# Kernel tuning notes

Hardware: AMD Instinct MI355X
Metric: run time of the kernel (lower is better)

Reference implementation:

```python
import jax, jax.numpy as jnp
import numpy as np

B, S, D, H = 2, 2048, 1024, 16
HD = D // H  # 64


def setup_inputs() -> dict:
    key = jax.random.key(0)
    ks = jax.random.split(key, 7)
    scale = 1.0 / np.sqrt(D)
    return {
        "embeddings": jax.random.normal(ks[0], (B, S, D), dtype=jnp.float32),
        "W_kv": jax.random.uniform(ks[1], (D, 2 * D), jnp.float32, -scale, scale),
        "b_kv": jax.random.uniform(ks[2], (2 * D,), jnp.float32, -scale, scale),
        "W_q": jax.random.uniform(ks[3], (D, D), jnp.float32, -scale, scale),
        "b_q": jax.random.uniform(ks[4], (D,), jnp.float32, -scale, scale),
        "W_o": jax.random.uniform(ks[5], (D, D), jnp.float32, -scale, scale),
        "b_o": jax.random.uniform(ks[6], (D,), jnp.float32, -scale, scale),
    }


def reference(embeddings, W_kv, b_kv, W_q, b_q, W_o, b_o):
    # kv projection -> [B, S, H, 2*HD] -> [B, H, S, 2*HD]
    kv = (embeddings @ W_kv + b_kv).reshape(B, S, H, 2 * HD).transpose(0, 2, 1, 3)
    q = (embeddings @ W_q + b_q).reshape(B, S, H, HD).transpose(0, 2, 1, 3)
    k, v = kv[..., :HD], kv[..., HD:]
    # naive scaled dot-product attention (full [B,H,S,S] score matrix)
    scores = jnp.einsum("bhqd,bhkd->bhqk", q, k) / jnp.sqrt(jnp.float32(HD))
    attn = jax.nn.softmax(scores, axis=-1)
    ctx = jnp.einsum("bhqk,bhkd->bhqd", attn, v)  # [B,H,S,HD]
    ctx = ctx.transpose(0, 2, 1, 3).reshape(B, S, D)
    return ctx @ W_o + b_o
```

## Files before the change

kernel.cpp:

```cpp
#include <hip/hip_runtime.h>
#include <hip/hip_bf16.h>


typedef unsigned short ushort;
typedef __attribute__((ext_vector_type(4))) float f32x4;
typedef __attribute__((ext_vector_type(16))) float f32x16;
typedef __attribute__((ext_vector_type(8))) __bf16 bf16x8;
typedef __attribute__((ext_vector_type(8))) unsigned short u16x8;
typedef __attribute__((ext_vector_type(4))) unsigned short u16x4;
typedef __attribute__((ext_vector_type(4))) unsigned int u32x4;

#define LOG2E 1.44269504088896340736f

constexpr int Bc = 2, Sc = 2048, Dc = 1024, Hc = 16, HDc = 64;

__device__ inline ushort f2bf(float f) {
    unsigned u = __builtin_bit_cast(unsigned, f);
    u += 0x7fffu + ((u >> 16) & 1u);
    return (ushort)(u >> 16);
}

__device__ inline float fexp2(float x) {
#if __has_builtin(__builtin_amdgcn_exp2f)
    return __builtin_amdgcn_exp2f(x);
#else
    return exp2f(x);
#endif
}

__device__ inline void gload16(const void* g, void* l) {
    __builtin_amdgcn_global_load_lds((const __attribute__((address_space(1))) void*)g,
                                     (__attribute__((address_space(3))) void*)l, 16, 0, 0);
}

__device__ inline f32x4 mfma16(bf16x8 a, bf16x8 b, f32x4 c) {
    return __builtin_amdgcn_mfma_f32_16x16x32_bf16(a, b, c, 0, 0, 0);
}
__device__ inline f32x16 mfma32(bf16x8 a, bf16x8 b, f32x16 c) {
    return __builtin_amdgcn_mfma_f32_32x32x16_bf16(a, b, c, 0, 0, 0);
}
__device__ inline unsigned cvtpk(float lo, float hi_) {
    unsigned r; asm("v_cvt_pk_bf16_f32 %0, %1, %2" : "=v"(r) : "v"(lo), "v"(hi_)); return r;
}
__device__ inline void swap32(unsigned& a, unsigned& b) {
    asm("v_permlane32_swap_b32 %0, %1" : "+v"(a), "+v"(b));
}

__global__ __launch_bounds__(256) void prep_k(const float* __restrict__ emb,
                                              ushort* __restrict__ embb,
                                              const float* __restrict__ Wkv,
                                              const float* __restrict__ Wq,
                                              const float* __restrict__ Wo,
                                              ushort* __restrict__ WtAll) {
    const int bid = blockIdx.x;
    if (bid < 2048) {
        int i = bid * 256 + threadIdx.x;
        const float4* p = (const float4*)emb;
        float4 a = p[2 * i], b = p[2 * i + 1];
        u16x8 r;
        r[0] = f2bf(a.x); r[1] = f2bf(a.y); r[2] = f2bf(a.z); r[3] = f2bf(a.w);
        r[4] = f2bf(b.x); r[5] = f2bf(b.y); r[6] = f2bf(b.z); r[7] = f2bf(b.w);
        ((u16x8*)embb)[i] = r;
        return;
    }
    __shared__ float t[32][33];
    int tb = bid - 2048;
    const float* W; int N, rowofs;
    if (tb < 2048)      { W = Wkv; N = 2048; rowofs = 0; }
    else if (tb < 3072) { W = Wq;  N = 1024; rowofs = 2048; tb -= 2048; }
    else                { W = Wo;  N = 1024; rowofs = 3072; tb -= 3072; }
    const int nbx = N >> 5;
    const int bx = tb % nbx, by = tb / nbx;
    const int tx = threadIdx.x & 31, ty = threadIdx.x >> 5;
    const int bj = bx * 32, bi = by * 32;
#pragma unroll
    for (int i = 0; i < 4; i++) {
        int r = ty + i * 8;
        t[r][tx] = W[(size_t)(bi + r) * N + bj + tx];
    }
    __syncthreads();
#pragma unroll
    for (int i = 0; i < 4; i++) {
        int r = ty + i * 8;
        WtAll[(size_t)(rowofs + bj + r) * 1024 + bi + tx] = f2bf(t[tx][r]);
    }
}

__global__ __launch_bounds__(512, 2) void gemm256_kv_k(const ushort* __restrict__ A,
                                                       const ushort* __restrict__ Bt,
                                                       const float* __restrict__ bias,
                                                       const float* __restrict__ bias2,
                                                       ushort* __restrict__ Kout,
                                                       ushort* __restrict__ Vout,
                                                       ushort* __restrict__ Qout,
                                                       int N, int K) {
    __shared__ __align__(16) char sA[2][32768];
    __shared__ __align__(16) char sB[2][32768];
    const int tid = threadIdx.x;
    const int nbc = N >> 8;
    const int cpx = (gridDim.x >> 3);
    const int swzb = (blockIdx.x & 7) * cpx + (blockIdx.x >> 3);
    const int brow = swzb / nbc, bcol = swzb % nbc;
    const int w = tid >> 6, lane = tid & 63;
    const int wr = w >> 2, wc = w & 3;
    const int lg = lane >> 4, l16 = lane & 15;

    f32x4 acc[8][4] = {};

    const int srow = tid >> 3;
    const int schunk = (tid & 7) ^ (srow & 7);
    const ushort* aP[4];
    const ushort* bP[4];
#pragma unroll
    for (int s = 0; s < 4; s++) {
        aP[s] = A  + (size_t)(brow * 256 + s * 64 + srow) * K + schunk * 8;
        bP[s] = Bt + (size_t)(bcol * 256 + s * 64 + srow) * K + schunk * 8;
    }

    auto STAGE_ALL = [&](int buf, int k0) {
#pragma unroll
        for (int s = 0; s < 4; s++)
            gload16(aP[s] + k0, sA[buf] + s * 8192 + w * 1024);
#pragma unroll
        for (int s = 0; s < 4; s++)
            gload16(bP[s] + k0, sB[buf] + s * 8192 + w * 1024);
    };

    const int aro = wr * 128 + l16;
    const int bro = wc * 64 + l16;
    const int axor = l16 & 7;

    const int nk = K >> 6;
    STAGE_ALL(0, 0);

    for (int kt = 0; kt < nk; kt++) {
        const int buf = kt & 1;
        if (kt < nk - 1) {
            STAGE_ALL(buf ^ 1, (kt + 1) << 6);
            asm volatile("s_waitcnt vmcnt(8)" ::: "memory");
        } else {
            asm volatile("s_waitcnt vmcnt(0)" ::: "memory");
        }
        __builtin_amdgcn_s_barrier();
        __builtin_amdgcn_sched_barrier(0);

#pragma unroll
        for (int ks = 0; ks < 2; ks++) {
            bf16x8 af[8], bfr[4];
#pragma unroll
            for (int rf = 0; rf < 8; rf++)
                af[rf] = *(const bf16x8*)(sA[buf] + (aro + rf * 16) * 128 +
                                          ((((ks << 2) | lg) ^ axor) << 4));
#pragma unroll
            for (int cf = 0; cf < 4; cf++)
                bfr[cf] = *(const bf16x8*)(sB[buf] + (bro + cf * 16) * 128 +
                                           ((((ks << 2) | lg) ^ axor) << 4));
#pragma unroll
            for (int rf = 0; rf < 8; rf++)
#pragma unroll
                for (int cf = 0; cf < 4; cf++)
                    acc[rf][cf] = mfma16(af[rf], bfr[cf], acc[rf][cf]);
        }
        __builtin_amdgcn_s_barrier();
    }

#pragma unroll
    for (int cf = 0; cf < 4; cf++) {
        const int col = bcol * 256 + wc * 64 + cf * 16 + l16;
        if (col < 2048) {
            const float bv = bias[col];
            const int h = col >> 7, lo = col & 127;
#pragma unroll
            for (int rf = 0; rf < 8; rf++) {
                int row = brow * 256 + wr * 128 + rf * 16 + lg * 4;
                int b = row >> 11, s = row & 2047;
                if (lo < 64) {
#pragma unroll
                    for (int r = 0; r < 4; r++)
                        Kout[((size_t)(b * 16 + h) * 2048 + s + r) * 64 + lo] =
                            f2bf(acc[rf][cf][r] + bv);
                } else {
                    u16x4 pk;
#pragma unroll
                    for (int r = 0; r < 4; r++) pk[r] = f2bf(acc[rf][cf][r] + bv);
                    *(u16x4*)(Vout + ((size_t)(b * 16 + h) * 64 + (lo - 64)) * 2048 + s) = pk;
                }
            }
        } else {
            const int qc = col - 2048;
            const float bv = bias2[qc];
            const float qs = 0.125f * LOG2E;
#pragma unroll
            for (int rf = 0; rf < 8; rf++) {
                int row = brow * 256 + wr * 128 + rf * 16 + lg * 4;
#pragma unroll
                for (int r = 0; r < 4; r++)
                    Qout[(size_t)(row + r) * 1024 + qc] =
                        f2bf((acc[rf][cf][r] + bv) * qs);
            }
        }
    }
}

template <int MODE>
__global__ __launch_bounds__(256) void gemm_bt_k(const ushort* __restrict__ A,
                                                 const ushort* __restrict__ Bt,
                                                 const float* __restrict__ bias,
                                                 void* __restrict__ Cout,
                                                 int M, int N, int K) {
    __shared__ __align__(16) char sA[2][8192];
    __shared__ __align__(16) char sB[2][8192];
    const int tid = threadIdx.x;
    const int nbc = N >> 7;
    const int cpx = (gridDim.x >> 3);
    const int swzb = (blockIdx.x & 7) * cpx + (blockIdx.x >> 3);
    const int brow = swzb / nbc, bcol = swzb % nbc;
    const int w = tid >> 6, lane = tid & 63;
    const int wr = w >> 1, wc = w & 1;
    const int lg = lane >> 4, l16 = lane & 15;

    f32x4 acc[4][4] = {};

    const int r0 = tid >> 2;
    const int sl = (tid & 3) ^ (r0 & 3);
    const ushort* a0 = A + (size_t)(brow * 128 + r0) * K + sl * 8;
    const ushort* a1 = A + (size_t)(brow * 128 + 64 + r0) * K + sl * 8;
    const ushort* b0 = Bt + (size_t)(bcol * 128 + r0) * K + sl * 8;
    const ushort* b1 = Bt + (size_t)(bcol * 128 + 64 + r0) * K + sl * 8;

    const int arow = wr * 64 + l16;
    const int bcolr = wc * 64 + l16;

    auto STAGE = [&](int buf, int k0) {
        gload16(a0 + k0, sA[buf] + w * 1024);
        gload16(a1 + k0, sA[buf] + 4096 + w * 1024);
        gload16(b0 + k0, sB[buf] + w * 1024);
        gload16(b1 + k0, sB[buf] + 4096 + w * 1024);
    };

    const int nk = K >> 5;
    STAGE(0, 0);

    for (int k0 = 0; k0 < nk; k0++) {
        const int buf = k0 & 1;
        if (k0 < nk - 1) {
            STAGE(buf ^ 1, (k0 + 1) << 5);
            asm volatile("s_waitcnt vmcnt(4)" ::: "memory");
        } else {
            asm volatile("s_waitcnt vmcnt(0)" ::: "memory");
        }
        __builtin_amdgcn_s_barrier();
        __builtin_amdgcn_sched_barrier(0);

        bf16x8 af[4], bfr[4];
#pragma unroll
        for (int rf = 0; rf < 4; rf++) {
            int rr = arow + rf * 16;
            af[rf] = *(const bf16x8*)(sA[buf] + rr * 64 + ((lg * 16) ^ ((rr & 3) << 4)));
        }
#pragma unroll
        for (int cf = 0; cf < 4; cf++) {
            int rr = bcolr + cf * 16;
            bfr[cf] = *(const bf16x8*)(sB[buf] + rr * 64 + ((lg * 16) ^ ((rr & 3) << 4)));
        }
#pragma unroll
        for (int rf = 0; rf < 4; rf++)
#pragma unroll
            for (int cf = 0; cf < 4; cf++)
                acc[rf][cf] = mfma16(af[rf], bfr[cf], acc[rf][cf]);
        __builtin_amdgcn_s_barrier();
    }

#pragma unroll
    for (int cf = 0; cf < 4; cf++) {
        const int col = bcol * 128 + wc * 64 + cf * 16 + l16;
        const float bv = bias[col];
#pragma unroll
        for (int rf = 0; rf < 4; rf++) {
            int row = brow * 128 + wr * 64 + rf * 16 + lg * 4;
#pragma unroll
            for (int r = 0; r < 4; r++) {
                float v = acc[rf][cf][r] + bv;
                if (MODE == 1) ((float*)Cout)[(size_t)(row + r) * N + col] = v;
                else           ((ushort*)Cout)[(size_t)(row + r) * N + col] = f2bf(v);
            }
        }
    }
}

__global__ __launch_bounds__(256, 2) void attn2_k(const ushort* __restrict__ Qg,
                                                  const ushort* __restrict__ Kg,
                                                  const ushort* __restrict__ Vg,
                                                  ushort* __restrict__ ctx) {
    __shared__ __align__(16) char sK[2][8192];
    __shared__ __align__(16) char sV[2][8192];
    __shared__ float lx2[256];
    const int tid = threadIdx.x;
    const int wg = ((blockIdx.x & 7) << 6) | (blockIdx.x >> 3);
    const int bh = wg >> 4, qt = wg & 15;
    const int b = bh >> 4, h = bh & 15;
    const int w = tid >> 6, lane = tid & 63;
    const int ql = lane & 31, hi = lane >> 5;
    const int ksub = w & 1;
    const int qq = w >> 1;

    const ushort* Kh = Kg + (size_t)bh * (Sc * 64);
    const ushort* Vh = Vg + (size_t)bh * (64 * Sc);

    const int qrow0 = qt * 128 + qq * 64 + ql;
    bf16x8 qf[2][4];
#pragma unroll
    for (int qg = 0; qg < 2; qg++) {
        const ushort* qp = Qg + ((size_t)(b * Sc + qrow0 + qg * 32)) * Dc + h * HDc + hi * 8;
#pragma unroll
        for (int jd = 0; jd < 4; jd++) qf[qg][jd] = *(const bf16x8*)(qp + jd * 16);
    }

    const u16x8 ones_u = {0x3F80, 0x3F80, 0x3F80, 0x3F80, 0x3F80, 0x3F80, 0x3F80, 0x3F80};
    const bf16x8 ones8 = __builtin_bit_cast(bf16x8, ones_u);

    const int rw = w * 16 + (lane >> 3);
    const int sl = (lane & 7) ^ (lane >> 3);

    f32x16 o[2][2] = {};
    f32x16 ls[2] = {};
    const float MH = 8.0f * LOG2E;
    const int sw = (ql & 7) << 4;

    auto STAGE = [&](int buf, int kt) {
#pragma unroll
        for (int j = 0; j < 2; j++) {
            gload16(Kh + (size_t)(kt * 64 + rw + 8 * j) * 64 + sl * 8,
                    sK[buf] + w * 2048 + j * 1024);
            gload16(Vh + (size_t)(rw + 8 * j) * Sc + kt * 64 + sl * 8,
                    sV[buf] + w * 2048 + j * 1024);
        }
    };

    int cur = 0;
    STAGE(0, 0);

    constexpr int NT = Sc / 64;
    for (int kt = 0; kt < NT; kt++) {
        if (kt < NT - 1) {
            STAGE(cur ^ 1, kt + 1);
            asm volatile("s_waitcnt vmcnt(4)" ::: "memory");
        } else {
            asm volatile("s_waitcnt vmcnt(0)" ::: "memory");
        }
        __builtin_amdgcn_s_barrier();
        __builtin_amdgcn_sched_barrier(0);

        bf16x8 kf[4];
        {
            const char* kb = sK[cur] + (ksub * 32 + ql) * 128;
#pragma unroll
            for (int jd = 0; jd < 4; jd++)
                kf[jd] = *(const bf16x8*)(kb + ((jd * 32 + hi * 16) ^ sw));
        }

        f32x16 st[2];
#pragma unroll
        for (int qg = 0; qg < 2; qg++)
#pragma unroll
            for (int i = 0; i < 16; i++) st[qg][i] = -MH;
        __builtin_amdgcn_s_setprio(1);
#pragma unroll
        for (int qg = 0; qg < 2; qg++)
#pragma unroll
            for (int jd = 0; jd < 4; jd++)
                st[qg] = mfma32(kf[jd], qf[qg][jd], st[qg]);
        __builtin_amdgcn_s_setprio(0);

#pragma unroll
        for (int qg = 0; qg < 2; qg++)
#pragma unroll
            for (int i = 0; i < 16; i++) st[qg][i] = fexp2(st[qg][i]);

        bf16x8 pf[2][2];
#pragma unroll
        for (int qg = 0; qg < 2; qg++) {
            unsigned a0 = cvtpk(st[qg][0],  st[qg][1]);
            unsigned a1 = cvtpk(st[qg][2],  st[qg][3]);
            unsigned a2 = cvtpk(st[qg][4],  st[qg][5]);
            unsigned a3 = cvtpk(st[qg][6],  st[qg][7]);
            swap32(a0, a2); swap32(a1, a3);
            u32x4 f0v = {a0, a1, a2, a3};
            pf[qg][0] = __builtin_bit_cast(bf16x8, f0v);
            unsigned c0 = cvtpk(st[qg][8],  st[qg][9]);
            unsigned c1 = cvtpk(st[qg][10], st[qg][11]);
            unsigned c2 = cvtpk(st[qg][12], st[qg][13]);
            unsigned c3 = cvtpk(st[qg][14], st[qg][15]);
            swap32(c0, c2); swap32(c1, c3);
            u32x4 f1v = {c0, c1, c2, c3};
            pf[qg][1] = __builtin_bit_cast(bf16x8, f1v);
        }

        bf16x8 vf[2][2];
#pragma unroll
        for (int dg = 0; dg < 2; dg++) {
            const char* vb = sV[cur] + (dg * 32 + ql) * 128;
#pragma unroll
            for (int ks = 0; ks < 2; ks++)
                vf[dg][ks] = *(const bf16x8*)(vb + ((ksub * 64 + ks * 32 + hi * 16) ^ sw));
        }

        __builtin_amdgcn_s_setprio(1);
#pragma unroll
        for (int qg = 0; qg < 2; qg++)
#pragma unroll
            for (int ks = 0; ks < 2; ks++) {
                o[0][qg] = mfma32(vf[0][ks], pf[qg][ks], o[0][qg]);
                o[1][qg] = mfma32(vf[1][ks], pf[qg][ks], o[1][qg]);
                ls[qg]   = mfma32(ones8,     pf[qg][ks], ls[qg]);
            }
        __builtin_amdgcn_s_setprio(0);

        __builtin_amdgcn_s_barrier();
        cur ^= 1;
    }

    __syncthreads();
    float* ox = qq ? (float*)sV : (float*)sK;
    if (ksub) {
#pragma unroll
        for (int dg = 0; dg < 2; dg++)
#pragma unroll
            for (int qg = 0; qg < 2; qg++)
#pragma unroll
                for (int i = 0; i < 16; i++)
                    ox[((dg * 2 + qg) * 16 + i) * 64 + lane] = o[dg][qg][i];
        lx2[(qq * 2 + 0) * 64 + lane] = ls[0][0];
        lx2[(qq * 2 + 1) * 64 + lane] = ls[1][0];
    }
    __syncthreads();
    if (!ksub) {
#pragma unroll
        for (int dg = 0; dg < 2; dg++)
#pragma unroll
            for (int qg = 0; qg < 2; qg++)
#pragma unroll
                for (int i = 0; i < 16; i++)
                    o[dg][qg][i] += ox[((dg * 2 + qg) * 16 + i) * 64 + lane];
        const float inv0 = 1.0f / (ls[0][0] + lx2[(qq * 2 + 0) * 64 + lane]);
        const float inv1 = 1.0f / (ls[1][0] + lx2[(qq * 2 + 1) * 64 + lane]);
#pragma unroll
        for (int qg = 0; qg < 2; qg++) {
            const float inv = qg ? inv1 : inv0;
            ushort* cp = ctx + ((size_t)(b * Sc + qrow0 + qg * 32)) * Dc + h * HDc;
#pragma unroll
            for (int dg = 0; dg < 2; dg++)
#pragma unroll
                for (int g = 0; g < 4; g++) {
                    u16x4 pk;
#pragma unroll
                    for (int r = 0; r < 4; r++)
                        pk[r] = f2bf(o[dg][qg][g * 4 + r] * inv);
                    *(u16x4*)(cp + dg * 32 + g * 8 + hi * 4) = pk;
                }
        }
    }
}

extern "C" void kernel_launch(void* const* d_in, const int* in_sizes, int n_in,
                              void* d_out, int out_size, void* d_ws, size_t ws_size,
                              hipStream_t stream) {
    const float* emb  = (const float*)d_in[0];
    const float* W_kv = (const float*)d_in[1];
    const float* b_kv = (const float*)d_in[2];
    const float* W_q  = (const float*)d_in[3];
    const float* b_q  = (const float*)d_in[4];
    const float* W_o  = (const float*)d_in[5];
    const float* b_o  = (const float*)d_in[6];
    float* out = (float*)d_out;

    const int BS = Bc * Sc;
    ushort* embb  = (ushort*)d_ws;
    ushort* wallt = embb  + (size_t)BS * Dc;
    ushort* wot   = wallt + (size_t)3 * Dc * Dc;
    ushort* Kb    = wallt + (size_t)4 * Dc * Dc;
    ushort* Vtb   = Kb    + (size_t)32 * Sc * HDc;
    ushort* Qb    = Vtb   + (size_t)32 * Sc * HDc;
    ushort* ctxb  = Qb    + (size_t)BS * Dc;

    prep_k<<<6144, 256, 0, stream>>>(emb, embb, W_kv, W_q, W_o, wallt);

    gemm256_kv_k<<<(BS / 256) * (3072 / 256), 512, 0, stream>>>(
        embb, wallt, b_kv, b_q, Kb, Vtb, Qb, 3072, Dc);

    attn2_k<<<Bc * Hc * (Sc / 128), 256, 0, stream>>>(Qb, Kb, Vtb, ctxb);

    gemm_bt_k<1><<<(BS / 128) * (Dc / 128), 256, 0, stream>>>(
        ctxb, wot, b_o, out, BS, Dc, Dc);
}
```

Measured before the change: 118.9 us.

## Restructure QKV GEMM mainloop into 8-phase quarter-tile ping-pong pipeline

The 256x256 QKV projection GEMM's main loop is split into four sub-phases, each working on half of A and half of B. In each phase the LDS fragment loads, the global-to-LDS prefetch for a quarter tile two iterations ahead, and a block of MFMAs are interleaved, with s_setprio around the MFMA groups. This aims to hide global load latency and LDS reads behind matrix math instead of stalling at one barrier per k-tile. In exchange there are many more barriers and tricky buffer reuse: quarters of the current buffer are overwritten while other quarters are still being consumed, which relies on careful ordering.

Measured after the change: 119.1 us. About the same (+0.1%).

```diff
diff --git a/kernel.cpp b/kernel.cpp
--- a/kernel.cpp
+++ b/kernel.cpp
@@ -86,14 +86,14 @@
     }
 }
 
-__global__ __launch_bounds__(512, 2) void gemm256_kv_k(const ushort* __restrict__ A,
-                                                       const ushort* __restrict__ Bt,
-                                                       const float* __restrict__ bias,
-                                                       const float* __restrict__ bias2,
-                                                       ushort* __restrict__ Kout,
-                                                       ushort* __restrict__ Vout,
-                                                       ushort* __restrict__ Qout,
-                                                       int N, int K) {
+__global__ __launch_bounds__(512, 2) void gemm256_kv8_k(const ushort* __restrict__ A,
+                                                        const ushort* __restrict__ Bt,
+                                                        const float* __restrict__ bias,
+                                                        const float* __restrict__ bias2,
+                                                        ushort* __restrict__ Kout,
+                                                        ushort* __restrict__ Vout,
+                                                        ushort* __restrict__ Qout,
+                                                        int N, int K) {
     __shared__ __align__(16) char sA[2][32768];
     __shared__ __align__(16) char sB[2][32768];
     const int tid = threadIdx.x;
@@ -104,64 +104,103 @@
     const int w = tid >> 6, lane = tid & 63;
     const int wr = w >> 2, wc = w & 3;
     const int lg = lane >> 4, l16 = lane & 15;
+    const int lx7 = l16 & 7;
 
     f32x4 acc[8][4] = {};
 
-    const int srow = tid >> 3;
-    const int schunk = (tid & 7) ^ (srow & 7);
-    const ushort* aP[4];
-    const ushort* bP[4];
-#pragma unroll
-    for (int s = 0; s < 4; s++) {
-        aP[s] = A  + (size_t)(brow * 256 + s * 64 + srow) * K + schunk * 8;
-        bP[s] = Bt + (size_t)(bcol * 256 + s * 64 + srow) * K + schunk * 8;
-    }
-
-    auto STAGE_ALL = [&](int buf, int k0) {
-#pragma unroll
-        for (int s = 0; s < 4; s++)
-            gload16(aP[s] + k0, sA[buf] + s * 8192 + w * 1024);
-#pragma unroll
-        for (int s = 0; s < 4; s++)
-            gload16(bP[s] + k0, sB[buf] + s * 8192 + w * 1024);
-    };
-
-    const int aro = wr * 128 + l16;
-    const int bro = wc * 64 + l16;
-    const int axor = l16 & 7;
+    const int srow8 = lane >> 3;
+    const int sch = (lane & 7) ^ srow8;
+    const ushort* Ab = A  + (size_t)(brow * 256 + w * 8 + srow8) * K + sch * 8;
+    const ushort* Bb = Bt + (size_t)(bcol * 256 + (w >> 2) * 64 + (w & 3) * 8 + srow8) * K + sch * 8;
+
+    auto ST_A = [&](int buf, int mh, int k0) {
+#pragma unroll
+        for (int j = 0; j < 2; j++)
+            gload16(Ab + (size_t)(j * 128 + mh * 64) * K + k0,
+                    sA[buf] + mh * 16384 + j * 8192 + w * 1024);
+    };
+    auto ST_B = [&](int buf, int nh, int k0) {
+#pragma unroll
+        for (int j = 0; j < 2; j++)
+            gload16(Bb + (size_t)(j * 128 + nh * 32) * K + k0,
+                    sB[buf] + nh * 16384 + j * 8192 + w * 1024);
+    };
+
+    bf16x8 af[4][2], bfr[2][2];
+    auto LD_A = [&](int buf, int mh) {
+#pragma unroll
+        for (int rf = 0; rf < 4; rf++)
+#pragma unroll
+            for (int ks = 0; ks < 2; ks++)
+                af[rf][ks] = *(const bf16x8*)(sA[buf] + mh * 16384 + wr * 8192 +
+                             (rf * 16 + l16) * 128 + ((((ks << 2) | lg) ^ lx7) << 4));
+    };
+    auto LD_B = [&](int buf, int nh) {
+#pragma unroll
+        for (int cf = 0; cf < 2; cf++)
+#pragma unroll
+            for (int ks = 0; ks < 2; ks++)
+                bfr[cf][ks] = *(const bf16x8*)(sB[buf] + nh * 16384 + wc * 4096 +
+                              (cf * 16 + l16) * 128 + ((((ks << 2) | lg) ^ lx7) << 4));
+    };
+    auto MMA = [&](int mh, int nh) {
+        __builtin_amdgcn_s_setprio(1);
+#pragma unroll
+        for (int rf = 0; rf < 4; rf++)
+#pragma unroll
+            for (int cf = 0; cf < 2; cf++)
+#pragma unroll
+                for (int ks = 0; ks < 2; ks++)
+                    acc[mh * 4 + rf][nh * 2 + cf] =
+                        mfma16(af[rf][ks], bfr[cf][ks], acc[mh * 4 + rf][nh * 2 + cf]);
+        __builtin_amdgcn_s_setprio(0);
+    };
 
     const int nk = K >> 6;
-    STAGE_ALL(0, 0);
+    ST_A(0, 0, 0);  ST_B(0, 1, 0);  ST_A(0, 1, 0);  ST_B(0, 0, 0);
+    ST_A(1, 0, 64); ST_B(1, 1, 64); ST_A(1, 1, 64);
+    asm volatile("s_waitcnt vmcnt(6)" ::: "memory");
+    __builtin_amdgcn_s_barrier();
+    __builtin_amdgcn_sched_barrier(0);
 
     for (int kt = 0; kt < nk; kt++) {
         const int buf = kt & 1;
-        if (kt < nk - 1) {
-            STAGE_ALL(buf ^ 1, (kt + 1) << 6);
-            asm volatile("s_waitcnt vmcnt(8)" ::: "memory");
-        } else {
-            asm volatile("s_waitcnt vmcnt(0)" ::: "memory");
-        }
-        __builtin_amdgcn_s_barrier();
-        __builtin_amdgcn_sched_barrier(0);
-
-#pragma unroll
-        for (int ks = 0; ks < 2; ks++) {
-            bf16x8 af[8], bfr[4];
-#pragma unroll
-            for (int rf = 0; rf < 8; rf++)
-                af[rf] = *(const bf16x8*)(sA[buf] + (aro + rf * 16) * 128 +
-                                          ((((ks << 2) | lg) ^ axor) << 4));
-#pragma unroll
-            for (int cf = 0; cf < 4; cf++)
-                bfr[cf] = *(const bf16x8*)(sB[buf] + (bro + cf * 16) * 128 +
-                                           ((((ks << 2) | lg) ^ axor) << 4));
-#pragma unroll
-            for (int rf = 0; rf < 8; rf++)
-#pragma unroll
-                for (int cf = 0; cf < 4; cf++)
-                    acc[rf][cf] = mfma16(af[rf], bfr[cf], acc[rf][cf]);
-        }
-        __builtin_amdgcn_s_barrier();
+        const int k2 = (kt + 2) << 6;
+        LD_A(buf, 0); LD_B(buf, 0);
+        if (kt < nk - 1) ST_B(buf ^ 1, 0, (kt + 1) << 6);
+        asm volatile("s_waitcnt lgkmcnt(8)" ::: "memory");
+        __builtin_amdgcn_s_barrier();
+        asm volatile("s_waitcnt lgkmcnt(0)" ::: "memory");
+        __builtin_amdgcn_sched_barrier(0);
+        MMA(0, 0);
+        __builtin_amdgcn_s_barrier();
+        __builtin_amdgcn_sched_barrier(0);
+        LD_B(buf, 1);
+        if (kt < nk - 2) ST_A(buf, 0, k2);
+        __builtin_amdgcn_s_barrier();
+        asm volatile("s_waitcnt lgkmcnt(0)" ::: "memory");
+        __builtin_amdgcn_sched_barrier(0);
+        MMA(0, 1);
+        __builtin_amdgcn_s_barrier();
+        __builtin_amdgcn_sched_barrier(0);
+        LD_A(buf, 1);
+        if (kt < nk - 2) ST_B(buf, 1, k2);
+        __builtin_amdgcn_s_barrier();
+        asm volatile("s_waitcnt lgkmcnt(0)" ::: "memory");
+        __builtin_amdgcn_sched_barrier(0);
+        MMA(1, 1);
+        __builtin_amdgcn_s_barrier();
+        __builtin_amdgcn_sched_barrier(0);
+        LD_B(buf, 0);
+        if (kt < nk - 2) ST_A(buf, 1, k2);
+        __builtin_amdgcn_s_barrier();
+        asm volatile("s_waitcnt lgkmcnt(0)" ::: "memory");
+        __builtin_amdgcn_sched_barrier(0);
+        MMA(1, 0);
+        if (kt < nk - 2)       asm volatile("s_waitcnt vmcnt(6)" ::: "memory");
+        else if (kt == nk - 2) asm volatile("s_waitcnt vmcnt(0)" ::: "memory");
+        __builtin_amdgcn_s_barrier();
+        __builtin_amdgcn_sched_barrier(0);
     }
 
 #pragma unroll
@@ -485,7 +524,7 @@
 
     prep_k<<<6144, 256, 0, stream>>>(emb, embb, W_kv, W_q, W_o, wallt);
 
-    gemm256_kv_k<<<(BS / 256) * (3072 / 256), 512, 0, stream>>>(
+    gemm256_kv8_k<<<(BS / 256) * (3072 / 256), 512, 0, stream>>>(
         embb, wallt, b_kv, b_q, Kb, Vtb, Qb, 3072, Dc);
 
     attn2_k<<<Bc * Hc * (Sc / 128), 256, 0, stream>>>(Qb, Kb, Vtb, ctxb);
```
